# Optimization experiments

Hardware: AMD Instinct MI355X
Metric: run time of the kernel (lower is better)

Reference implementation:

```python
import jax, jax.numpy as jnp
import numpy as np

B, S, HID = 1, 2048, 2048
NH, NKV = 32, 8
HD = HID // NH  # 64
WINDOW = 1024
ROPE_BASE = 500000.0


def setup_inputs() -> dict:
    key = jax.random.key(0)
    ks = jax.random.split(key, 5)
    sc = 0.02
    return {
        "hidden_states": jax.random.normal(ks[0], (B, S, HID), dtype=jnp.float32),
        "Wq": jax.random.normal(ks[1], (HID, NH * HD), dtype=jnp.float32) * sc,
        "Wk": jax.random.normal(ks[2], (HID, NKV * HD), dtype=jnp.float32) * sc,
        "Wv": jax.random.normal(ks[3], (HID, NKV * HD), dtype=jnp.float32) * sc,
        "Wo": jax.random.normal(ks[4], (NH * HD, HID), dtype=jnp.float32) * sc,
    }


def _rope_cos_sin(seq_len, dtype):
    inv_freq = 1.0 / (ROPE_BASE ** (jnp.arange(0, HD, 2, dtype=jnp.float32) / HD))
    pos = jnp.arange(seq_len, dtype=jnp.float32)
    freqs = pos[:, None] * inv_freq[None, :]          # [S, HD/2]
    emb = jnp.concatenate([freqs, freqs], axis=-1)    # [S, HD]
    return jnp.cos(emb).astype(dtype), jnp.sin(emb).astype(dtype)


def _rotate_half(x):
    x1, x2 = x[..., : HD // 2], x[..., HD // 2:]
    return jnp.concatenate([-x2, x1], axis=-1)


def reference(hidden_states, Wq, Wk, Wv, Wo):
    b, s, _ = hidden_states.shape
    q = (hidden_states @ Wq).reshape(b, s, NH, HD).transpose(0, 2, 1, 3)   # [B,NH,S,D]
    k = (hidden_states @ Wk).reshape(b, s, NKV, HD).transpose(0, 2, 1, 3)  # [B,NKV,S,D]
    v = (hidden_states @ Wv).reshape(b, s, NKV, HD).transpose(0, 2, 1, 3)

    cos, sin = _rope_cos_sin(s, hidden_states.dtype)  # [S, D]
    cos, sin = cos[None, None], sin[None, None]       # [1,1,S,D]
    q = q * cos + _rotate_half(q) * sin
    k = k * cos + _rotate_half(k) * sin

    n_rep = NH // NKV
    k = jnp.repeat(k, n_rep, axis=1)  # [B,NH,S,D]
    v = jnp.repeat(v, n_rep, axis=1)

    # sliding-window causal additive mask
    row = jnp.arange(s)[:, None]
    col = jnp.arange(s)[None, :]
    banned = (col > row) | (col < row - WINDOW + 1)
    mask = jnp.where(banned, jnp.float32(-jnp.inf), 0.0).astype(hidden_states.dtype)

    scale = 1.0 / np.sqrt(HD)
    scores = jnp.einsum("bhqd,bhkd->bhqk", q, k) * scale + mask
    attn = jax.nn.softmax(scores, axis=-1)
    out = jnp.einsum("bhqk,bhkd->bhqd", attn, v)          # [B,NH,S,D]
    out = out.transpose(0, 2, 1, 3).reshape(b, s, NH * HD)
    return out @ Wo
```

## Files before the change

### kernel.cpp

```cpp
#include <hip/hip_runtime.h>
#include <hip/hip_bf16.h>
#include <math.h>

#define S_LEN 2048
#define HID 2048
#define NH 32
#define NKV 8
#define HD 64
#define WINDOW 1024
#define QBLK 128
#define QKVN 3072

typedef __attribute__((ext_vector_type(8))) short bx8;
typedef __attribute__((ext_vector_type(4))) float fx4;
typedef __attribute__((ext_vector_type(8))) unsigned short us8;

#define GL_LDS16(gp, lp) \
    __builtin_amdgcn_global_load_lds((__attribute__((address_space(1))) const void*)(gp), \
                                     (__attribute__((address_space(3))) void*)(lp), 16, 0, 0)


__global__ __launch_bounds__(256) void prep_kernel(const float* __restrict__ hs,
                                                   const float* __restrict__ Wq,
                                                   const float* __restrict__ Wk,
                                                   const float* __restrict__ Wv,
                                                   const float* __restrict__ Wo,
                                                   float* __restrict__ cosT, float* __restrict__ sinT,
                                                   __hip_bfloat16* __restrict__ hsb,
                                                   __hip_bfloat16* __restrict__ WqkvT,
                                                   __hip_bfloat16* __restrict__ WoT) {
    __shared__ float tile[32][33];
    int b = blockIdx.x, t = threadIdx.x;
    if (b < 256) {
        int idx = b * 256 + t;
        int s = idx >> 5, f = idx & 31;
        double inv = exp(-2.0 * (double)f / 64.0 * log(500000.0));
        double ang = (double)s * inv;
        cosT[idx] = (float)cos(ang);
        sinT[idx] = (float)sin(ang);
        return;
    }
    b -= 256;
    if (b < 2048) {
        const int r = t >> 2, sl = t & 3;
        const int mt = b >> 6, kt = b & 63;
        const int chunk = sl ^ ((r >> 1) & 3);
        const float* src = &hs[(size_t)(mt * 64 + r) * 2048 + kt * 32 + chunk * 8];
        float4 a = *reinterpret_cast<const float4*>(src);
        float4 c = *reinterpret_cast<const float4*>(src + 4);
        __hip_bfloat16 o[8] __attribute__((aligned(16)));
        o[0] = __float2bfloat16(a.x); o[1] = __float2bfloat16(a.y);
        o[2] = __float2bfloat16(a.z); o[3] = __float2bfloat16(a.w);
        o[4] = __float2bfloat16(c.x); o[5] = __float2bfloat16(c.y);
        o[6] = __float2bfloat16(c.z); o[7] = __float2bfloat16(c.w);
        *reinterpret_cast<bx8*>(&hsb[(size_t)b * 2048 + t * 8]) = *reinterpret_cast<bx8*>(o);
        return;
    }
    b -= 2048;
    const float* src; __hip_bfloat16* dst; int Nd, bx, by, gbase;
    if (b < 4096)      { src = Wq; dst = WqkvT; Nd = 2048; bx = b & 63; by = b >> 6; gbase = 0; }
    else if (b < 5120) { b -= 4096; src = Wk; dst = WqkvT; Nd = 512; bx = b & 15; by = b >> 4; gbase = 2048; }
    else if (b < 6144) { b -= 5120; src = Wv; dst = WqkvT; Nd = 512; bx = b & 15; by = b >> 4; gbase = 2560; }
    else               { b -= 6144; src = Wo; dst = WoT;   Nd = 2048; bx = b & 63; by = b >> 6; gbase = 0; }
    int n0 = bx * 32, k0 = by * 32, tx = t & 31, ty = t >> 5;
#pragma unroll
    for (int i = 0; i < 4; i++)
        tile[ty + 8 * i][tx] = src[(size_t)(k0 + ty + 8 * i) * Nd + n0 + tx];
    __syncthreads();
    const int kt = k0 >> 5, chunk = tx >> 3, ko = tx & 7;
#pragma unroll
    for (int i = 0; i < 4; i++) {
        int gn = gbase + n0 + ty + 8 * i;
        int nt = gn >> 7, r = gn & 127;
        int s2 = chunk ^ ((r >> 1) & 3);
        dst[(size_t)(nt * 64 + kt) * 4096 + r * 32 + s2 * 8 + ko] =
            __float2bfloat16(tile[tx][ty + 8 * i]);
    }
}

__global__ __launch_bounds__(256) void ropev_kernel(__hip_bfloat16* __restrict__ QKV,
                                                    __hip_bfloat16* __restrict__ Vt,
                                                    const float* __restrict__ cosT,
                                                    const float* __restrict__ sinT) {
    __shared__ __hip_bfloat16 tile[32][33];
    int b = blockIdx.x, t = threadIdx.x;
    if (b < 10240) {
        int idx = b * 256 + t;
        int f = idx & 31;
        int head = (idx >> 5) % (NH + NKV);
        int s = idx / ((NH + NKV) * 32);
        float c  = cosT[(s << 5) + f];
        float sn = sinT[(s << 5) + f];
        __hip_bfloat16* p = (head < NH) ? (QKV + (size_t)s * QKVN + head * HD)
                                        : (QKV + (size_t)s * QKVN + 2048 + (head - NH) * HD);
        float x1 = __bfloat162float(p[f]), x2 = __bfloat162float(p[f + 32]);
        p[f]      = __float2bfloat16(x1 * c - x2 * sn);
        p[f + 32] = __float2bfloat16(x2 * c + x1 * sn);
        return;
    }
    b -= 10240;
    int s0 = (b & 63) * 32, d0 = (b >> 6) * 32;
    int tx = t & 31, ty = t >> 5;
#pragma unroll
    for (int i = 0; i < 4; i++)
        tile[ty + 8 * i][tx] = QKV[(size_t)(s0 + ty + 8 * i) * QKVN + 2560 + d0 + tx];
    __syncthreads();
#pragma unroll
    for (int i = 0; i < 4; i++)
        Vt[(size_t)(d0 + ty + 8 * i) * S_LEN + s0 + tx] = tile[tx][ty + 8 * i];
}

template <int APACKED, int OUTBF16>
__global__ __launch_bounds__(256) void gemm_pipe_kernel(const __hip_bfloat16* __restrict__ A,
                                                        const __hip_bfloat16* __restrict__ Bpk,
                                                        void* __restrict__ Cp,
                                                        int M, int N, int K, int stripe) {
    __shared__ __hip_bfloat16 As[4][2048];
    __shared__ __hip_bfloat16 Bs[4][4096];

    const int bid = blockIdx.x;
    const int x = bid & 7, j = bid >> 3;
    const int bn = (x * stripe + j % stripe) * 128;
    const int bm = (j / stripe) * 64;

    const int t = threadIdx.x, w = t >> 6, l = t & 63;
    const int wr = (w >> 1) * 32, wc = (w & 1) * 64;
    const int lr = l & 15;
    const int rdslot = (((l >> 4) ^ ((lr >> 1) & 3))) * 8;
    const int srow = w * 16 + (l >> 2);
    const int scol = (((l & 3) ^ ((l >> 3) & 3))) * 8;
    const int ldsoff = w * 512;

    const __hip_bfloat16* ga0 = APACKED
        ? A + (size_t)(bm >> 6) * 131072 + t * 8
        : A + (size_t)(bm + srow) * K + scol;
    const __hip_bfloat16* gb0 = Bpk + (size_t)(bn >> 7) * 262144 + t * 8;

    fx4 acc[2][4];
#pragma unroll
    for (int m = 0; m < 2; m++)
#pragma unroll
        for (int n = 0; n < 4; n++) acc[m][n] = (fx4){0.f, 0.f, 0.f, 0.f};

    const int T = K >> 5;

#define STAGE(kt, b)                                                      \
    do {                                                                  \
        const __hip_bfloat16* ga = APACKED ? ga0 + (kt) * 2048            \
                                           : ga0 + (kt) * 32;             \
        const __hip_bfloat16* gb = gb0 + (kt) * 4096;                     \
        GL_LDS16(ga,        &As[(b)][ldsoff]);                            \
        GL_LDS16(gb,        &Bs[(b)][ldsoff]);                            \
        GL_LDS16(gb + 2048, &Bs[(b)][2048 + ldsoff]);                     \
    } while (0)

    STAGE(0, 0);
    STAGE(1, 1);
    STAGE(2, 2);

    for (int i = 0; i < T; i++) {
        const int r = i & 3;
        if (i + 2 < T)      asm volatile("s_waitcnt vmcnt(6)" ::: "memory");
        else if (i + 1 < T) asm volatile("s_waitcnt vmcnt(3)" ::: "memory");
        else                asm volatile("s_waitcnt vmcnt(0)" ::: "memory");
        __builtin_amdgcn_s_barrier();
        asm volatile("" ::: "memory");
        if (i + 3 < T) STAGE(i + 3, (i + 3) & 3);

        bx8 af[2], bf[4];
#pragma unroll
        for (int m = 0; m < 2; m++)
            af[m] = *reinterpret_cast<const bx8*>(&As[r][(wr + m * 16 + lr) * 32 + rdslot]);
#pragma unroll
        for (int n = 0; n < 4; n++)
            bf[n] = *reinterpret_cast<const bx8*>(&Bs[r][(wc + n * 16 + lr) * 32 + rdslot]);
#pragma unroll
        for (int m = 0; m < 2; m++)
#pragma unroll
            for (int n = 0; n < 4; n++)
                acc[m][n] = __builtin_amdgcn_mfma_f32_16x16x32_bf16(af[m], bf[n], acc[m][n], 0, 0, 0);
    }
#undef STAGE

    const int lq = (l >> 4) * 4;
#pragma unroll
    for (int m = 0; m < 2; m++)
#pragma unroll
        for (int n = 0; n < 4; n++)
#pragma unroll
            for (int r2 = 0; r2 < 4; r2++) {
                int row = bm + wr + m * 16 + lq + r2;
                int col = bn + wc + n * 16 + lr;
                float v = acc[m][n][r2];
                if (OUTBF16)
                    ((__hip_bfloat16*)Cp)[(size_t)row * N + col] = __float2bfloat16(v);
                else
                    ((float*)Cp)[(size_t)row * N + col] = v;
            }
}

__global__ __launch_bounds__(512, 4) void attn_kernel(const __hip_bfloat16* __restrict__ Q,
                                                      const __hip_bfloat16* __restrict__ Kg,
                                                      const __hip_bfloat16* __restrict__ Vtg,
                                                      __hip_bfloat16* __restrict__ Ab) {
    __shared__ __hip_bfloat16 Ks[2][4096];
    __shared__ __hip_bfloat16 Vs[2][4096];
    __shared__ __hip_bfloat16 Ps[QBLK * 64];

    const int bid = blockIdx.x;
    const int swz = (bid & 7) * 64 + (bid >> 3);
    const int h = swz >> 4, qi = swz & 15;
    const int qb = qi * QBLK;
    const int kvh = h >> 2;

    const int t = threadIdx.x, w = t >> 6, l = t & 63;
    const int lr = l & 15, g = l >> 4, lk = g * 8;
    const int qbw = qb + 16 * w;
    const int prow = 16 * w + lr;
    const int psz = (prow & 7) << 4;

    char* PsB = (char*)Ps;

    bx8 qa[2];
#pragma unroll
    for (int ks = 0; ks < 2; ks++)
        qa[ks] = *reinterpret_cast<const bx8*>(
            &Q[(size_t)(qbw + lr) * QKVN + h * HD + ks * 32 + lk]);

    fx4 ot[4];
#pragma unroll
    for (int n = 0; n < 4; n++) ot[n] = (fx4){0.f, 0.f, 0.f, 0.f};
    float mrow = -1e30f, srow = 0.f;

    const int k0_first = (qb >= 1024) ? (qb - 1024) : 0;
    const int k0_last  = qb + 64;
    const int wmax = qbw + 15;
    const int wlow = qbw - (WINDOW - 1);
    const int rowq = qbw + lr;

    const int sr = t >> 3, c8 = t & 7;
    const int scolsw = 8 * (c8 ^ (sr & 7));
    const int kcol = kvh * HD + scolsw;
    const int vrow = kvh * HD + sr;
    __hip_bfloat16* ldsK = &Ks[0][0] + (t >> 6) * 512;
    __hip_bfloat16* ldsV = &Vs[0][0] + (t >> 6) * 512;

#define ASTAGE(k0v, p)                                                           \
    do {                                                                         \
        GL_LDS16(&Kg[(size_t)((k0v) + sr) * QKVN + kcol], ldsK + (p) * 4096);    \
        GL_LDS16(&Vtg[(size_t)vrow * S_LEN + (k0v) + scolsw], ldsV + (p) * 4096);\
    } while (0)

    ASTAGE(k0_first, 0);

    int ti = 0;
    for (int k0 = k0_first; k0 <= k0_last; k0 += 64, ++ti) {
        const int p = ti & 1;
        asm volatile("s_waitcnt vmcnt(0)" ::: "memory");
        __builtin_amdgcn_s_barrier();
        asm volatile("" ::: "memory");
        if (k0 + 64 <= k0_last) ASTAGE(k0 + 64, p ^ 1);

        if (k0 <= wmax && k0 + 63 >= wlow) {
            char* KsB = (char*)&Ks[p][0];
            char* VsB = (char*)&Vs[p][0];
            bx8 kb[4][2];
#pragma unroll
            for (int n = 0; n < 4; n++)
#pragma unroll
                for (int ks = 0; ks < 2; ks++) {
                    int row = 16 * n + lr;
                    kb[n][ks] = *reinterpret_cast<const bx8*>(
                        KsB + row * 128 + (((ks * 64) + 16 * g) ^ ((row & 7) << 4)));
                }
            fx4 sc[4];
#pragma unroll
            for (int n = 0; n < 4; n++) {
                sc[n] = __builtin_amdgcn_mfma_f32_16x16x32_bf16(kb[n][0], qa[0],
                                                                (fx4){0.f, 0.f, 0.f, 0.f}, 0, 0, 0);
                sc[n] = __builtin_amdgcn_mfma_f32_16x16x32_bf16(kb[n][1], qa[1], sc[n], 0, 0, 0);
            }
            const bool interior = (k0 + 63 <= qbw) && (k0 >= qbw - 1008);
            if (interior) {
#pragma unroll
                for (int n = 0; n < 4; n++)
#pragma unroll
                    for (int r = 0; r < 4; r++) sc[n][r] *= 0.125f;
            } else {
#pragma unroll
                for (int n = 0; n < 4; n++)
#pragma unroll
                    for (int r = 0; r < 4; r++) {
                        int key = k0 + 16 * n + 4 * g + r;
                        bool valid = (key <= rowq) && (key >= rowq - (WINDOW - 1));
                        sc[n][r] = valid ? sc[n][r] * 0.125f : -1e30f;
                    }
            }
            float tmax = fmaxf(fmaxf(sc[0][0], sc[0][1]), fmaxf(sc[0][2], sc[0][3]));
#pragma unroll
            for (int n = 1; n < 4; n++)
                tmax = fmaxf(tmax, fmaxf(fmaxf(sc[n][0], sc[n][1]), fmaxf(sc[n][2], sc[n][3])));
            tmax = fmaxf(tmax, __shfl_xor(tmax, 16));
            tmax = fmaxf(tmax, __shfl_xor(tmax, 32));
            const bool grew = __any(tmax > mrow);
            float mn = mrow, fs = 1.f;
            if (grew) {
                mn = fmaxf(mrow, tmax);
                fs = __expf(mrow - mn);
                mrow = mn;
            }
            float ps = 0.f;
#pragma unroll
            for (int n = 0; n < 4; n++) {
#pragma unroll
                for (int r = 0; r < 4; r++) {
                    float p2 = __expf(sc[n][r] - mn);
                    sc[n][r] = p2;
                    ps += p2;
                }
                __hip_bfloat16 pk[4] __attribute__((aligned(8)));
                pk[0] = __float2bfloat16(sc[n][0]); pk[1] = __float2bfloat16(sc[n][1]);
                pk[2] = __float2bfloat16(sc[n][2]); pk[3] = __float2bfloat16(sc[n][3]);
                *reinterpret_cast<unsigned long long*>(PsB + prow * 128 + ((32 * n + 8 * g) ^ psz)) =
                    *reinterpret_cast<unsigned long long*>(pk);
            }
            ps += __shfl_xor(ps, 16);
            ps += __shfl_xor(ps, 32);
            if (grew) {
                srow = srow * fs + ps;
#pragma unroll
                for (int n = 0; n < 4; n++)
#pragma unroll
                    for (int r = 0; r < 4; r++) ot[n][r] *= fs;
            } else {
                srow += ps;
            }
            bx8 vb[4][2];
#pragma unroll
            for (int n = 0; n < 4; n++)
#pragma unroll
                for (int ks = 0; ks < 2; ks++) {
                    int row = 16 * n + lr;
                    vb[n][ks] = *reinterpret_cast<const bx8*>(
                        VsB + row * 128 + (((ks * 64) + 16 * g) ^ ((row & 7) << 4)));
                }
            bx8 pb[2];
#pragma unroll
            for (int ks = 0; ks < 2; ks++)
                pb[ks] = *reinterpret_cast<const bx8*>(
                    PsB + prow * 128 + (((ks * 64) + 16 * g) ^ psz));
#pragma unroll
            for (int n = 0; n < 4; n++) {
                ot[n] = __builtin_amdgcn_mfma_f32_16x16x32_bf16(vb[n][0], pb[0], ot[n], 0, 0, 0);
                ot[n] = __builtin_amdgcn_mfma_f32_16x16x32_bf16(vb[n][1], pb[1], ot[n], 0, 0, 0);
            }
        }
    }
#undef ASTAGE

    const float inv = 1.f / srow;
#pragma unroll
    for (int n = 0; n < 4; n++) {
        __hip_bfloat16 pk[4] __attribute__((aligned(8)));
#pragma unroll
        for (int r = 0; r < 4; r++) pk[r] = __float2bfloat16(ot[n][r] * inv);
        *reinterpret_cast<unsigned long long*>(PsB + prow * 128 + ((32 * n + 8 * g) ^ psz)) =
            *reinterpret_cast<unsigned long long*>(pk);
    }
    __syncthreads();
#pragma unroll
    for (int j = 0; j < 2; j++) {
        const int row = (t >> 3) + 64 * j, c = t & 7;
        us8 v = *reinterpret_cast<const us8*>(PsB + row * 128 + ((c * 16) ^ ((row & 7) << 4)));
        *reinterpret_cast<us8*>(&Ab[(size_t)(qb + row) * HID + h * HD + c * 8]) = v;
    }
}

extern "C" void kernel_launch(void* const* d_in, const int* in_sizes, int n_in,
                              void* d_out, int out_size, void* d_ws, size_t ws_size,
                              hipStream_t stream) {
    const float* hs = (const float*)d_in[0];
    const float* Wq = (const float*)d_in[1];
    const float* Wk = (const float*)d_in[2];
    const float* Wv = (const float*)d_in[3];
    const float* Wo = (const float*)d_in[4];

    float* ws   = (float*)d_ws;
    float* cosT = ws;
    float* sinT = cosT + 65536;
    __hip_bfloat16* hsb    = (__hip_bfloat16*)(sinT + 65536);
    __hip_bfloat16* WqkvT  = hsb + 4194304;
    __hip_bfloat16* WoT    = WqkvT + 6291456;
    __hip_bfloat16* QKVb   = WoT + 4194304;
    __hip_bfloat16* Vt     = QKVb + 6291456;
    __hip_bfloat16* Ab     = hsb;

    prep_kernel<<<12544, 256, 0, stream>>>(hs, Wq, Wk, Wv, Wo, cosT, sinT, hsb, WqkvT, WoT);

    gemm_pipe_kernel<1, 1><<<768, 256, 0, stream>>>(hsb, WqkvT, QKVb, 2048, QKVN, 2048, 3);

    ropev_kernel<<<11264, 256, 0, stream>>>(QKVb, Vt, cosT, sinT);

    attn_kernel<<<512, 512, 0, stream>>>(QKVb, QKVb + 2048, Vt, Ab);

    gemm_pipe_kernel<0, 0><<<512, 256, 0, stream>>>(Ab, WoT, d_out, 2048, 2048, 2048, 2);
}
```

Measured before the change: 144.0 us.

## Fuse RoPE into QKV GEMM epilogue and write attention output pre-packed

The QKV projection GEMM now applies RoPE in its epilogue for Q and K columns. Each wave's 64-column slice is exactly one head, so the two halves being rotated sit in the same thread's accumulators. This removes the separate elementwise pass that read and rewrote Q/K in global memory, leaving a small V-transpose kernel. The attention kernel also writes its output straight into the swizzled packed tile layout, so the output GEMM can use its packed-A load path. The cost is extra cos/sin loads in the GEMM epilogue and tighter coupling between the attention store and the GEMM's layout.

```diff
diff --git a/kernel.cpp b/kernel.cpp
--- a/kernel.cpp
+++ b/kernel.cpp
@@ -78,27 +78,10 @@
     }
 }
 
-__global__ __launch_bounds__(256) void ropev_kernel(__hip_bfloat16* __restrict__ QKV,
-                                                    __hip_bfloat16* __restrict__ Vt,
-                                                    const float* __restrict__ cosT,
-                                                    const float* __restrict__ sinT) {
+__global__ __launch_bounds__(256) void vtrans_kernel(const __hip_bfloat16* __restrict__ QKV,
+                                                     __hip_bfloat16* __restrict__ Vt) {
     __shared__ __hip_bfloat16 tile[32][33];
     int b = blockIdx.x, t = threadIdx.x;
-    if (b < 10240) {
-        int idx = b * 256 + t;
-        int f = idx & 31;
-        int head = (idx >> 5) % (NH + NKV);
-        int s = idx / ((NH + NKV) * 32);
-        float c  = cosT[(s << 5) + f];
-        float sn = sinT[(s << 5) + f];
-        __hip_bfloat16* p = (head < NH) ? (QKV + (size_t)s * QKVN + head * HD)
-                                        : (QKV + (size_t)s * QKVN + 2048 + (head - NH) * HD);
-        float x1 = __bfloat162float(p[f]), x2 = __bfloat162float(p[f + 32]);
-        p[f]      = __float2bfloat16(x1 * c - x2 * sn);
-        p[f + 32] = __float2bfloat16(x2 * c + x1 * sn);
-        return;
-    }
-    b -= 10240;
     int s0 = (b & 63) * 32, d0 = (b >> 6) * 32;
     int tx = t & 31, ty = t >> 5;
 #pragma unroll
@@ -110,10 +93,12 @@
         Vt[(size_t)(d0 + ty + 8 * i) * S_LEN + s0 + tx] = tile[tx][ty + 8 * i];
 }
 
-template <int APACKED, int OUTBF16>
+template <int APACKED, int OUTBF16, int ROPE>
 __global__ __launch_bounds__(256) void gemm_pipe_kernel(const __hip_bfloat16* __restrict__ A,
                                                         const __hip_bfloat16* __restrict__ Bpk,
                                                         void* __restrict__ Cp,
+                                                        const float* __restrict__ cosT,
+                                                        const float* __restrict__ sinT,
                                                         int M, int N, int K, int stripe) {
     __shared__ __hip_bfloat16 As[4][2048];
     __shared__ __hip_bfloat16 Bs[4][4096];
@@ -183,20 +168,31 @@
 #undef STAGE
 
     const int lq = (l >> 4) * 4;
+    const bool doRope = ROPE && (bn + wc) < 2560;
 #pragma unroll
     for (int m = 0; m < 2; m++)
 #pragma unroll
-        for (int n = 0; n < 4; n++)
-#pragma unroll
-            for (int r2 = 0; r2 < 4; r2++) {
-                int row = bm + wr + m * 16 + lq + r2;
-                int col = bn + wc + n * 16 + lr;
-                float v = acc[m][n][r2];
+        for (int r2 = 0; r2 < 4; r2++) {
+            const int row = bm + wr + m * 16 + lq + r2;
+            float v0 = acc[m][0][r2], v1 = acc[m][1][r2];
+            float v2 = acc[m][2][r2], v3 = acc[m][3][r2];
+            if (doRope) {
+                float c0 = cosT[(row << 5) + lr],      s0 = sinT[(row << 5) + lr];
+                float c1 = cosT[(row << 5) + 16 + lr], s1 = sinT[(row << 5) + 16 + lr];
+                float o0 = v0 * c0 - v2 * s0, o2 = v2 * c0 + v0 * s0;
+                float o1 = v1 * c1 - v3 * s1, o3 = v3 * c1 + v1 * s1;
+                v0 = o0; v1 = o1; v2 = o2; v3 = o3;
+            }
+            float vv[4] = {v0, v1, v2, v3};
+#pragma unroll
+            for (int n = 0; n < 4; n++) {
+                int col = bn + wc + 16 * n + lr;
                 if (OUTBF16)
-                    ((__hip_bfloat16*)Cp)[(size_t)row * N + col] = __float2bfloat16(v);
+                    ((__hip_bfloat16*)Cp)[(size_t)row * N + col] = __float2bfloat16(vv[n]);
                 else
-                    ((float*)Cp)[(size_t)row * N + col] = v;
-            }
+                    ((float*)Cp)[(size_t)row * N + col] = vv[n];
+            }
+        }
 }
 
 __global__ __launch_bounds__(512, 4) void attn_kernel(const __hip_bfloat16* __restrict__ Q,
@@ -372,7 +368,11 @@
     for (int j = 0; j < 2; j++) {
         const int row = (t >> 3) + 64 * j, c = t & 7;
         us8 v = *reinterpret_cast<const us8*>(PsB + row * 128 + ((c * 16) ^ ((row & 7) << 4)));
-        *reinterpret_cast<us8*>(&Ab[(size_t)(qb + row) * HID + h * HD + c * 8]) = v;
+        const int R = qb + row;
+        const int mt = R >> 6, rloc = R & 63;
+        const int kt = 2 * h + (c >> 2);
+        const int slot = (c & 3) ^ ((rloc >> 1) & 3);
+        *reinterpret_cast<us8*>(&Ab[(size_t)(mt * 64 + kt) * 2048 + rloc * 32 + slot * 8]) = v;
     }
 }
 
@@ -397,11 +397,13 @@
 
     prep_kernel<<<12544, 256, 0, stream>>>(hs, Wq, Wk, Wv, Wo, cosT, sinT, hsb, WqkvT, WoT);
 
-    gemm_pipe_kernel<1, 1><<<768, 256, 0, stream>>>(hsb, WqkvT, QKVb, 2048, QKVN, 2048, 3);
-
-    ropev_kernel<<<11264, 256, 0, stream>>>(QKVb, Vt, cosT, sinT);
+    gemm_pipe_kernel<1, 1, 1><<<768, 256, 0, stream>>>(hsb, WqkvT, QKVb, cosT, sinT,
+                                                       2048, QKVN, 2048, 3);
+
+    vtrans_kernel<<<1024, 256, 0, stream>>>(QKVb, Vt);
 
     attn_kernel<<<512, 512, 0, stream>>>(QKVb, QKVb + 2048, Vt, Ab);
 
-    gemm_pipe_kernel<0, 0><<<512, 256, 0, stream>>>(Ab, WoT, d_out, 2048, 2048, 2048, 2);
+    gemm_pipe_kernel<1, 0, 0><<<512, 256, 0, stream>>>(Ab, WoT, d_out, nullptr, nullptr,
+                                                       2048, 2048, 2048, 2);
 }
```

Result: faster. 140.5 us (-2.4%).
